# Kernel tuning notes

Measured on AMD Instinct MI355X. Metric: run time of the kernel, lower is better.

Reference implementation:

```python
import jax, jax.numpy as jnp
import numpy as np

B, L_ENC, L_DEC, D = 16, 512, 128, 1024


def setup_inputs() -> dict:
    key = jax.random.key(0)
    k1, k2, k3, k4, k5, k6 = jax.random.split(key, 6)
    encoder_hc = jax.random.normal(k1, (B, L_ENC, D), dtype=jnp.float32)
    decoder_hq = jax.random.normal(k2, (B, L_DEC, D), dtype=jnp.float32)
    # linear_sim: Linear(3*D, 1) -> weight vector [3D] + scalar bias
    w_sim = jax.random.normal(k3, (3 * D,), dtype=jnp.float32) * 0.02
    b_sim = jax.random.normal(k4, (1,), dtype=jnp.float32) * 0.02
    # linear_QV: Linear(4*D, D); stored as [4D, D] so y = x @ W_qv + b_qv
    W_qv = jax.random.normal(k5, (4 * D, D), dtype=jnp.float32) * 0.02
    b_qv = jax.random.normal(k6, (D,), dtype=jnp.float32) * 0.02
    return {"encoder_hc": encoder_hc, "decoder_hq": decoder_hq,
            "w_sim": w_sim, "b_sim": b_sim, "W_qv": W_qv, "b_qv": b_qv}


def reference(encoder_hc, decoder_hq, w_sim, b_sim, W_qv, b_qv):
    d = encoder_hc.shape[-1]
    w1, w2, w3 = w_sim[:d], w_sim[d:2 * d], w_sim[2 * d:]
    # Fused trilinear similarity: Sim[b,i,j] = w1.hc_i + w2.hq_j + w3.(hc_i*hq_j) + b
    # (algebraically identical to linear_sim(cat[hc_i, hq_j, hc_i*hq_j]))
    Sim = ((encoder_hc @ w1)[:, :, None]            # [B, L_enc, 1]
           + (decoder_hq @ w2)[:, None, :]          # [B, 1, L_dec]
           + jnp.einsum('bid,bjd->bij', encoder_hc * w3, decoder_hq)
           + b_sim[0])                              # [B, L_enc, L_dec]
    # Context-to-query attention
    A = jax.nn.softmax(Sim, axis=2)
    hq_hat = jnp.einsum('bij,bjd->bid', A, decoder_hq)          # [B, L_enc, D]
    # Query-to-context attention (max over decoder positions)
    Batt = jax.nn.softmax(jnp.max(Sim, axis=2), axis=1)          # [B, L_enc]
    hc_bar = jnp.einsum('bi,bid->bd', Batt, encoder_hc)[:, None, :]  # [B, 1, D]
    hc_hat = jnp.broadcast_to(hc_bar, encoder_hc.shape)          # tiled over L_enc
    feats = jnp.concatenate(
        [encoder_hc, hq_hat, encoder_hc * hq_hat, encoder_hc * hc_hat], axis=-1)
    hcq = feats @ W_qv + b_qv                                    # [B, L_enc, D]
    return hcq
```

## Files before the change

### kernel.cpp

```cpp
#include <hip/hip_runtime.h>

#define DEV __device__ __forceinline__

typedef __bf16 bf16;
typedef __bf16 bf16x4 __attribute__((ext_vector_type(4)));
typedef __bf16 bf16x8 __attribute__((ext_vector_type(8)));
typedef float f32x4 __attribute__((ext_vector_type(4)));

constexpr int BB = 16, LE = 512, LD = 128, DD = 1024;
constexpr int MALL = BB * LE;
constexpr int K4 = 4 * DD;

constexpr size_t OFF_FEATS = 0;
constexpr size_t OFF_HQW3  = OFF_FEATS + (size_t)MALL * K4 * 2;
constexpr size_t OFF_HQT   = OFF_HQW3 + (size_t)BB * LD * DD * 2;
constexpr size_t OFF_WT    = OFF_HQT + (size_t)BB * DD * LD * 2;
constexpr size_t OFF_ABF   = OFF_WT + (size_t)K4 * DD * 2;
constexpr size_t OFF_S1    = OFF_ABF + (size_t)MALL * LD * 2;
constexpr size_t OFF_S2    = OFF_S1 + (size_t)MALL * 4;
constexpr size_t OFF_MROW  = OFF_S2 + (size_t)BB * LD * 4;
constexpr size_t OFF_HCBAR = OFF_MROW + (size_t)MALL * 4;

DEV void gload16(const void* g, void* l) {
  __builtin_amdgcn_global_load_lds(
      (const __attribute__((address_space(1))) void*)g,
      (__attribute__((address_space(3))) void*)l, 16, 0, 0);
}

__global__ __launch_bounds__(256) void k_prep(const float* __restrict__ hc,
                                              const float* __restrict__ hq,
                                              const float* __restrict__ wsim,
                                              bf16* __restrict__ feats,
                                              bf16* __restrict__ hqw3,
                                              float* __restrict__ s1,
                                              float* __restrict__ s2) {
  const int r = blockIdx.x;
  const int t = threadIdx.x;
  __shared__ float red[4];
  float dot;
  if (r < MALL) {
    const float4 v = reinterpret_cast<const float4*>(hc + (size_t)r * DD)[t];
    const float4 w = reinterpret_cast<const float4*>(wsim)[t];
    bf16x4 o; o[0] = (bf16)v.x; o[1] = (bf16)v.y; o[2] = (bf16)v.z; o[3] = (bf16)v.w;
    *reinterpret_cast<bf16x4*>(feats + (size_t)r * K4 + t * 4) = o;
    dot = v.x * w.x + v.y * w.y + v.z * w.z + v.w * w.w;
  } else {
    const int rw = r - MALL;
    const float4 v = reinterpret_cast<const float4*>(hq + (size_t)rw * DD)[t];
    const float4 w2 = reinterpret_cast<const float4*>(wsim + DD)[t];
    const float4 w3 = reinterpret_cast<const float4*>(wsim + 2 * DD)[t];
    bf16x4 o; o[0] = (bf16)(v.x * w3.x); o[1] = (bf16)(v.y * w3.y);
    o[2] = (bf16)(v.z * w3.z); o[3] = (bf16)(v.w * w3.w);
    *reinterpret_cast<bf16x4*>(hqw3 + (size_t)rw * DD + t * 4) = o;
    dot = v.x * w2.x + v.y * w2.y + v.z * w2.z + v.w * w2.w;
  }
  #pragma unroll
  for (int o = 32; o; o >>= 1) dot += __shfl_down(dot, o);
  const int lane = t & 63, w = t >> 6;
  if (lane == 0) red[w] = dot;
  __syncthreads();
  if (t == 0) {
    float s = red[0] + red[1] + red[2] + red[3];
    if (r < MALL) s1[r] = s; else s2[r - MALL] = s;
  }
}

__global__ __launch_bounds__(256) void k_transpose(const float* __restrict__ in,
                                                   bf16* __restrict__ out,
                                                   int R, int C, long ibs, long obs) {
  __shared__ float tile[64][68];
  const float* inp = in + (size_t)blockIdx.z * ibs;
  bf16* outp = out + (size_t)blockIdx.z * obs;
  const int r0 = blockIdx.y * 64, c0 = blockIdx.x * 64;
  const int t = threadIdx.x;
  #pragma unroll
  for (int i = 0; i < 4; i++) {
    const int r = i * 16 + (t >> 4), c = (t & 15) << 2;
    const float4 v = *reinterpret_cast<const float4*>(inp + (size_t)(r0 + r) * C + c0 + c);
    tile[r][c] = v.x; tile[r][c + 1] = v.y; tile[r][c + 2] = v.z; tile[r][c + 3] = v.w;
  }
  __syncthreads();
  {
    const int oc = t >> 2;
    const int g = t & 3;
    bf16x8 t0, t1;
    #pragma unroll
    for (int i = 0; i < 8; i++) t0[i] = (bf16)tile[g * 16 + i][oc];
    #pragma unroll
    for (int i = 0; i < 8; i++) t1[i] = (bf16)tile[g * 16 + 8 + i][oc];
    bf16* op = outp + (size_t)(c0 + oc) * R + r0 + g * 16;
    *reinterpret_cast<bf16x8*>(op) = t0;
    *reinterpret_cast<bf16x8*>(op + 8) = t1;
  }
}

template <int KTILES>
DEV void gemm_core(char* smem,
                   const bf16* __restrict__ Ag, int lda,
                   const bf16* __restrict__ Bg, int ldb,
                   f32x4 acc[4][4]) {
  bf16* As = (bf16*)smem;
  bf16* Bs = (bf16*)(smem + 16384);
  const int t = threadIdx.x;
  const int lane = t & 63;
  const int w = t >> 6;
  const int wm = w >> 1, wn = w & 1;
  const int l8 = lane >> 3, lc = lane & 7;
  const int ar = lane & 15;
  const int ak = (lane >> 4) * 8;
  const f32x4 zero = {0.f, 0.f, 0.f, 0.f};
  #pragma unroll
  for (int i = 0; i < 4; i++)
    #pragma unroll
    for (int j = 0; j < 4; j++) acc[i][j] = zero;

  for (int kt = 0; kt < KTILES; kt++) {
    const int k0 = kt * 64;
    #pragma unroll
    for (int c = 0; c < 4; c++) {
      const int row = c * 32 + w * 8 + l8;
      gload16(Ag + (size_t)row * lda + k0 + lc * 8, (char*)As + c * 4096 + w * 1024);
      gload16(Bg + (size_t)row * ldb + k0 + lc * 8, (char*)Bs + c * 4096 + w * 1024);
    }
    __syncthreads();
    #pragma unroll
    for (int kk = 0; kk < 2; kk++) {
      bf16x8 a[4], b[4];
      #pragma unroll
      for (int i = 0; i < 4; i++) {
        a[i] = *reinterpret_cast<const bf16x8*>(&As[(wm * 64 + i * 16 + ar) * 64 + kk * 32 + ak]);
        b[i] = *reinterpret_cast<const bf16x8*>(&Bs[(wn * 64 + i * 16 + ar) * 64 + kk * 32 + ak]);
      }
      #pragma unroll
      for (int i = 0; i < 4; i++)
        #pragma unroll
        for (int j = 0; j < 4; j++)
          acc[i][j] = __builtin_amdgcn_mfma_f32_16x16x32_bf16(a[i], b[j], acc[i][j], 0, 0, 0);
    }
    __syncthreads();
  }
}

__global__ __launch_bounds__(256) void k_sim(const bf16* __restrict__ feats,
                                             const bf16* __restrict__ hqw3,
                                             const float* __restrict__ s1,
                                             const float* __restrict__ s2,
                                             const float* __restrict__ bsim,
                                             bf16* __restrict__ Abf,
                                             float* __restrict__ mrow) {
  __shared__ __align__(16) char smem[128 * 129 * 4];
  __shared__ float invs[128];
  const int b = blockIdx.x, it = blockIdx.y;
  const int m0 = b * LE + it * 128;
  const int t = threadIdx.x;
  f32x4 acc[4][4];
  gemm_core<16>(smem, feats + (size_t)m0 * K4, K4, hqw3 + (size_t)b * LD * DD, DD, acc);

  float* simt = (float*)smem;
  const float bs = bsim[0];
  const int lane = t & 63, w = t >> 6, wm = w >> 1, wn = w & 1;
  #pragma unroll
  for (int i = 0; i < 4; i++)
    #pragma unroll
    for (int r = 0; r < 4; r++) {
      const int ml = wm * 64 + i * 16 + (lane >> 4) * 4 + r;
      const float s1v = s1[m0 + ml] + bs;
      #pragma unroll
      for (int j = 0; j < 4; j++) {
        const int nl = wn * 64 + j * 16 + (lane & 15);
        simt[ml * 129 + nl] = acc[i][j][r] + s1v + s2[b * LD + nl];
      }
    }
  __syncthreads();

  {
    const int row = t >> 1, half = t & 1;
    float* rp = simt + row * 129 + half * 64;
    float m = rp[0];
    #pragma unroll
    for (int k = 1; k < 64; k++) m = fmaxf(m, rp[k]);
    m = fmaxf(m, __shfl_xor(m, 1));
    float s = 0.f;
    #pragma unroll
    for (int k = 0; k < 64; k++) { const float e = __expf(rp[k] - m); rp[k] = e; s += e; }
    s += __shfl_xor(s, 1);
    if (half == 0) { invs[row] = 1.0f / s; mrow[m0 + row] = m; }
  }
  __syncthreads();

  #pragma unroll
  for (int it8 = 0; it8 < 8; it8++) {
    const int rr = it8 * 16 + (t >> 4), cc = (t & 15) * 8;
    const float iv = invs[rr];
    bf16x8 o;
    #pragma unroll
    for (int u = 0; u < 8; u++) o[u] = (bf16)(simt[rr * 129 + cc + u] * iv);
    *reinterpret_cast<bf16x8*>(Abf + (size_t)(m0 + rr) * LD + cc) = o;
  }
}

__global__ __launch_bounds__(256) void k_batt(const float* __restrict__ mrow,
                                              const float* __restrict__ hc,
                                              float* __restrict__ hcbar) {
  const int b = blockIdx.x, dc = blockIdx.y, t = threadIdx.x;
  __shared__ float batt[512];
  __shared__ float red[4];
  const int lane = t & 63, w = t >> 6;
  const float m0 = mrow[b * LE + t], m1 = mrow[b * LE + 256 + t];
  float m = fmaxf(m0, m1);
  #pragma unroll
  for (int o = 32; o; o >>= 1) m = fmaxf(m, __shfl_xor(m, o));
  if (lane == 0) red[w] = m;
  __syncthreads();
  m = fmaxf(fmaxf(red[0], red[1]), fmaxf(red[2], red[3]));
  const float e0 = __expf(m0 - m), e1 = __expf(m1 - m);
  float s = e0 + e1;
  #pragma unroll
  for (int o = 32; o; o >>= 1) s += __shfl_xor(s, o);
  __syncthreads();
  if (lane == 0) red[w] = s;
  __syncthreads();
  s = red[0] + red[1] + red[2] + red[3];
  const float inv = 1.0f / s;
  batt[t] = e0 * inv;
  batt[t + 256] = e1 * inv;
  __syncthreads();
  const int d = dc * 256 + t;
  float acc = 0.0f;
  const float* hcb = hc + (size_t)b * LE * DD + d;
  #pragma unroll 8
  for (int i = 0; i < LE; i++) acc += batt[i] * hcb[(size_t)i * DD];
  hcbar[b * DD + d] = acc;
}

__global__ __launch_bounds__(256) void k_hqhat(const bf16* __restrict__ Abf,
                                               const bf16* __restrict__ hqT,
                                               const float* __restrict__ hc,
                                               const float* __restrict__ hcbar,
                                               bf16* __restrict__ feats) {
  __shared__ __align__(16) char smem[128 * 136 * 2];
  const int b = blockIdx.x, it = blockIdx.y, nt = blockIdx.z;
  const int m0 = b * LE + it * 128;
  const int n0 = nt * 128;
  const int t = threadIdx.x;
  f32x4 acc[4][4];
  gemm_core<2>(smem, Abf + (size_t)m0 * LD, LD,
               hqT + (size_t)b * DD * LD + (size_t)n0 * LD, LD, acc);

  bf16* tile = (bf16*)smem;
  const int lane = t & 63, w = t >> 6, wm = w >> 1, wn = w & 1;
  #pragma unroll
  for (int i = 0; i < 4; i++)
    #pragma unroll
    for (int j = 0; j < 4; j++)
      #pragma unroll
      for (int r = 0; r < 4; r++) {
        const int ml = wm * 64 + i * 16 + (lane >> 4) * 4 + r;
        const int nl = wn * 64 + j * 16 + (lane & 15);
        tile[ml * 136 + nl] = (bf16)acc[i][j][r];
      }
  __syncthreads();

  const int d = n0 + (t & 15) * 8;
  const float4 hb0 = *reinterpret_cast<const float4*>(hcbar + b * DD + d);
  const float4 hb1 = *reinterpret_cast<const float4*>(hcbar + b * DD + d + 4);
  const float hbv[8] = {hb0.x, hb0.y, hb0.z, hb0.w, hb1.x, hb1.y, hb1.z, hb1.w};
  #pragma unroll
  for (int it8 = 0; it8 < 8; it8++) {
    const int rr = it8 * 16 + (t >> 4);
    const int m = m0 + rr;
    const bf16x8 hv = *reinterpret_cast<const bf16x8*>(&tile[rr * 136 + (t & 15) * 8]);
    const float4 c0 = *reinterpret_cast<const float4*>(hc + (size_t)m * DD + d);
    const float4 c1 = *reinterpret_cast<const float4*>(hc + (size_t)m * DD + d + 4);
    const float hcv[8] = {c0.x, c0.y, c0.z, c0.w, c1.x, c1.y, c1.z, c1.w};
    bf16x8 q2, q3;
    #pragma unroll
    for (int u = 0; u < 8; u++) {
      q2[u] = (bf16)(hcv[u] * (float)hv[u]);
      q3[u] = (bf16)(hcv[u] * hbv[u]);
    }
    bf16* f = feats + (size_t)m * K4;
    *reinterpret_cast<bf16x8*>(f + DD + d) = hv;
    *reinterpret_cast<bf16x8*>(f + 2 * DD + d) = q2;
    *reinterpret_cast<bf16x8*>(f + 3 * DD + d) = q3;
  }
}

__global__ __launch_bounds__(256) void k_final(const bf16* __restrict__ feats,
                                               const bf16* __restrict__ WT,
                                               const float* __restrict__ bqv,
                                               float* __restrict__ out) {
  __shared__ __align__(16) char smem[64 * 132 * 4];
  const int mt = blockIdx.x, nt = blockIdx.y;
  const int n0 = nt * 128;
  const int t = threadIdx.x;
  f32x4 acc[4][4];
  gemm_core<64>(smem, feats + (size_t)mt * 128 * K4, K4,
                WT + (size_t)n0 * K4, K4, acc);

  float* tile = (float*)smem;
  const int lane = t & 63, w = t >> 6, wm = w >> 1, wn = w & 1;
  const int cc = (t & 31) * 4;
  const float4 bq = *reinterpret_cast<const float4*>(bqv + n0 + cc);
  #pragma unroll
  for (int p = 0; p < 2; p++) {
    if (wm == p) {
      #pragma unroll
      for (int i = 0; i < 4; i++)
        #pragma unroll
        for (int j = 0; j < 4; j++)
          #pragma unroll
          for (int r = 0; r < 4; r++) {
            const int ml = i * 16 + (lane >> 4) * 4 + r;
            const int nl = wn * 64 + j * 16 + (lane & 15);
            tile[ml * 132 + nl] = acc[i][j][r];
          }
    }
    __syncthreads();
    #pragma unroll
    for (int itx = 0; itx < 8; itx++) {
      const int rr = itx * 8 + (t >> 5);
      const f32x4 v = *reinterpret_cast<const f32x4*>(&tile[rr * 132 + cc]);
      float4 o;
      o.x = v[0] + bq.x; o.y = v[1] + bq.y; o.z = v[2] + bq.z; o.w = v[3] + bq.w;
      *reinterpret_cast<float4*>(out + (size_t)(mt * 128 + p * 64 + rr) * DD + n0 + cc) = o;
    }
    __syncthreads();
  }
}

extern "C" void kernel_launch(void* const* d_in, const int* in_sizes, int n_in,
                              void* d_out, int out_size, void* d_ws, size_t ws_size,
                              hipStream_t stream) {
  const float* hc = (const float*)d_in[0];
  const float* hq = (const float*)d_in[1];
  const float* wsim = (const float*)d_in[2];
  const float* bsim = (const float*)d_in[3];
  const float* Wqv = (const float*)d_in[4];
  const float* bqv = (const float*)d_in[5];
  float* out = (float*)d_out;

  char* ws = (char*)d_ws;
  bf16* feats = (bf16*)(ws + OFF_FEATS);
  bf16* hqw3 = (bf16*)(ws + OFF_HQW3);
  bf16* hqT = (bf16*)(ws + OFF_HQT);
  bf16* WT = (bf16*)(ws + OFF_WT);
  bf16* Abf = (bf16*)(ws + OFF_ABF);
  float* s1 = (float*)(ws + OFF_S1);
  float* s2 = (float*)(ws + OFF_S2);
  float* mrow = (float*)(ws + OFF_MROW);
  float* hcbar = (float*)(ws + OFF_HCBAR);

  k_prep<<<MALL + BB * LD, 256, 0, stream>>>(hc, hq, wsim, feats, hqw3, s1, s2);
  k_transpose<<<dim3(DD / 64, LD / 64, BB), 256, 0, stream>>>(hq, hqT, LD, DD,
                                                              (long)LD * DD, (long)DD * LD);
  k_transpose<<<dim3(DD / 64, K4 / 64, 1), 256, 0, stream>>>(Wqv, WT, K4, DD, 0, 0);
  k_sim<<<dim3(BB, LE / 128), 256, 0, stream>>>(feats, hqw3, s1, s2, bsim, Abf, mrow);
  k_batt<<<dim3(BB, DD / 256), 256, 0, stream>>>(mrow, hc, hcbar);
  k_hqhat<<<dim3(BB, LE / 128, DD / 128), 256, 0, stream>>>(Abf, hqT, hc, hcbar, feats);
  k_final<<<dim3(MALL / 128, DD / 128), 256, 0, stream>>>(feats, WT, bqv, out);
}
```

Baseline: 278.5 us.

## Rewrite final GEMM with 256x128 tiles and triple-buffered LDS pipeline

Replaces the final feats@W_qv GEMM kernel with a 512-thread version that computes 256x128 output tiles. It triple-buffers XOR-swizzled LDS tiles, loaded via global_load_lds two k-steps ahead, and raises wave priority around the MFMA blocks. The goal is to hide global memory latency and reuse more data per block in the dominant GEMM. In exchange it uses 144KB of LDS per block and an explicit waitcnt/barrier schedule that is fragile if the counts are wrong.

```diff
diff --git a/kernel.cpp b/kernel.cpp
--- a/kernel.cpp
+++ b/kernel.cpp
@@ -286,24 +286,114 @@
   }
 }
 
-__global__ __launch_bounds__(256) void k_final(const bf16* __restrict__ feats,
-                                               const bf16* __restrict__ WT,
-                                               const float* __restrict__ bqv,
-                                               float* __restrict__ out) {
-  __shared__ __align__(16) char smem[64 * 132 * 4];
+__global__ __launch_bounds__(512, 2) void k_final2(const bf16* __restrict__ feats,
+                                                   const bf16* __restrict__ WT,
+                                                   const float* __restrict__ bqv,
+                                                   float* __restrict__ out) {
+  __shared__ __align__(16) char smem[3 * 49152];
   const int mt = blockIdx.x, nt = blockIdx.y;
-  const int n0 = nt * 128;
-  const int t = threadIdx.x;
+  const int t = threadIdx.x;
+  const int lane = t & 63, w = t >> 6;
+  const int wm = w >> 1, wn = w & 1;
+  const int l8 = lane >> 3, lc = lane & 7;
+  const int ar = lane & 15;
+  const int cg = lane >> 4;
+  const int a7 = lane & 7;
+  const int arow = w * 8 + l8;
+  const int schunk = (lc ^ l8) * 8;
+  const int w8 = w * 8;
+
+  const bf16* Ag = feats + (size_t)mt * 256 * K4;
+  const bf16* Bg = WT + (size_t)nt * 128 * K4;
+
   f32x4 acc[4][4];
-  gemm_core<64>(smem, feats + (size_t)mt * 128 * K4, K4,
-                WT + (size_t)n0 * K4, K4, acc);
+  const f32x4 zero = {0.f, 0.f, 0.f, 0.f};
+  #pragma unroll
+  for (int i = 0; i < 4; i++)
+    #pragma unroll
+    for (int j = 0; j < 4; j++) acc[i][j] = zero;
+
+  #define STAGE_A(base, c, k0) \
+    gload16(Ag + (size_t)((c) * 64 + arow) * K4 + (k0) + schunk, (base) + ((c) * 64 + w8) * 128)
+  #define STAGE_B(base, c, k0) \
+    gload16(Bg + (size_t)((c) * 64 + arow) * K4 + (k0) + schunk, (base) + 32768 + ((c) * 64 + w8) * 128)
+
+  #define LDA(base, i, kk) \
+    (*(const bf16x8*)((base) + (wm * 64 + (i) * 16 + ar) * 128 + (((kk) * 4 + cg) ^ a7) * 16))
+  #define LDB(base, j, kk) \
+    (*(const bf16x8*)((base) + 32768 + (wn * 64 + (j) * 16 + ar) * 128 + (((kk) * 4 + cg) ^ a7) * 16))
+
+  {
+    char* b0 = smem;
+    STAGE_A(b0, 0, 0); STAGE_A(b0, 1, 0); STAGE_A(b0, 2, 0); STAGE_A(b0, 3, 0);
+    STAGE_B(b0, 0, 0); STAGE_B(b0, 1, 0);
+    char* b1 = smem + 49152;
+    STAGE_A(b1, 0, 64); STAGE_A(b1, 1, 64); STAGE_A(b1, 2, 64); STAGE_A(b1, 3, 64);
+    STAGE_B(b1, 0, 64); STAGE_B(b1, 1, 64);
+  }
+  asm volatile("s_waitcnt vmcnt(6)" ::: "memory");
+  __builtin_amdgcn_s_barrier();
+
+  int rd = 0, st = 2;
+  for (int kt = 0; kt < 64; kt++) {
+    char* bA = smem + rd * 49152;
+    char* sA = smem + st * 49152;
+    const int k2 = (kt + 2) * 64;
+    const bool do_stage = (kt + 2) < 64;
+    bf16x8 a[4], b[4];
+
+    #pragma unroll
+    for (int i = 0; i < 4; i++) a[i] = LDA(bA, i, 0);
+    #pragma unroll
+    for (int j = 0; j < 4; j++) b[j] = LDB(bA, j, 0);
+    if (do_stage) { STAGE_A(sA, 0, k2); STAGE_A(sA, 1, k2); STAGE_B(sA, 0, k2); }
+    __builtin_amdgcn_s_barrier();
+    asm volatile("s_waitcnt lgkmcnt(0)" ::: "memory");
+    __builtin_amdgcn_sched_barrier(0);
+    __builtin_amdgcn_s_setprio(1);
+    #pragma unroll
+    for (int i = 0; i < 4; i++)
+      #pragma unroll
+      for (int j = 0; j < 4; j++)
+        acc[i][j] = __builtin_amdgcn_mfma_f32_16x16x32_bf16(a[i], b[j], acc[i][j], 0, 0, 0);
+    __builtin_amdgcn_s_setprio(0);
+    __builtin_amdgcn_s_barrier();
+
+    #pragma unroll
+    for (int i = 0; i < 4; i++) a[i] = LDA(bA, i, 1);
+    #pragma unroll
+    for (int j = 0; j < 4; j++) b[j] = LDB(bA, j, 1);
+    if (do_stage) { STAGE_A(sA, 2, k2); STAGE_A(sA, 3, k2); STAGE_B(sA, 1, k2); }
+    __builtin_amdgcn_s_barrier();
+    asm volatile("s_waitcnt lgkmcnt(0)" ::: "memory");
+    __builtin_amdgcn_sched_barrier(0);
+    __builtin_amdgcn_s_setprio(1);
+    #pragma unroll
+    for (int i = 0; i < 4; i++)
+      #pragma unroll
+      for (int j = 0; j < 4; j++)
+        acc[i][j] = __builtin_amdgcn_mfma_f32_16x16x32_bf16(a[i], b[j], acc[i][j], 0, 0, 0);
+    __builtin_amdgcn_s_setprio(0);
+    if (do_stage) asm volatile("s_waitcnt vmcnt(6)" ::: "memory");
+    else          asm volatile("s_waitcnt vmcnt(0)" ::: "memory");
+    __builtin_amdgcn_s_barrier();
+
+    rd = (rd == 2) ? 0 : rd + 1;
+    st = (st == 2) ? 0 : st + 1;
+  }
+  #undef STAGE_A
+  #undef STAGE_B
+  #undef LDA
+  #undef LDB
+
+  __builtin_amdgcn_sched_barrier(0);
 
   float* tile = (float*)smem;
-  const int lane = t & 63, w = t >> 6, wm = w >> 1, wn = w & 1;
   const int cc = (t & 31) * 4;
-  const float4 bq = *reinterpret_cast<const float4*>(bqv + n0 + cc);
-  #pragma unroll
-  for (int p = 0; p < 2; p++) {
+  const float4 bq = *reinterpret_cast<const float4*>(bqv + nt * 128 + cc);
+  __syncthreads();
+  #pragma unroll
+  for (int p = 0; p < 4; p++) {
     if (wm == p) {
       #pragma unroll
       for (int i = 0; i < 4; i++)
@@ -318,12 +408,12 @@
     }
     __syncthreads();
     #pragma unroll
-    for (int itx = 0; itx < 8; itx++) {
-      const int rr = itx * 8 + (t >> 5);
+    for (int itx = 0; itx < 4; itx++) {
+      const int rr = itx * 16 + (t >> 5);
       const f32x4 v = *reinterpret_cast<const f32x4*>(&tile[rr * 132 + cc]);
       float4 o;
       o.x = v[0] + bq.x; o.y = v[1] + bq.y; o.z = v[2] + bq.z; o.w = v[3] + bq.w;
-      *reinterpret_cast<float4*>(out + (size_t)(mt * 128 + p * 64 + rr) * DD + n0 + cc) = o;
+      *reinterpret_cast<float4*>(out + (size_t)(mt * 256 + p * 64 + rr) * DD + nt * 128 + cc) = o;
     }
     __syncthreads();
   }
@@ -358,5 +448,5 @@
   k_sim<<<dim3(BB, LE / 128), 256, 0, stream>>>(feats, hqw3, s1, s2, bsim, Abf, mrow);
   k_batt<<<dim3(BB, DD / 256), 256, 0, stream>>>(mrow, hc, hcbar);
   k_hqhat<<<dim3(BB, LE / 128, DD / 128), 256, 0, stream>>>(Abf, hqT, hc, hcbar, feats);
-  k_final<<<dim3(MALL / 128, DD / 128), 256, 0, stream>>>(feats, WT, bqv, out);
-}
+  k_final2<<<dim3(MALL / 256, DD / 128), 512, 0, stream>>>(feats, WT, bqv, out);
+}
```

New measurement: 248.1 us. 1.12x faster.
